# Kernel tuning notes

Hardware: AMD Instinct MI355X
Metric: run time of the kernel (lower is better)

## Reference

```python
import jax, jax.numpy as jnp
import numpy as np

DIM = 1024
EXP = 4           # expansion_factor
NUM_EXPERTS = 4
BATCH, SEQ = 4, 4096


def setup_inputs() -> dict:
    key = jax.random.key(0)
    ks = jax.random.split(key, 6)
    x = jax.random.normal(ks[0], (BATCH, SEQ, DIM), dtype=jnp.float32)
    token_mask = jax.random.randint(ks[1], (BATCH, SEQ), 0, NUM_EXPERTS, dtype=jnp.int32)
    hid = DIM * EXP
    s1 = 1.0 / np.sqrt(DIM)
    s2 = 1.0 / np.sqrt(hid)
    # nn.Linear layout: weight [out_features, in_features]
    w1 = jax.random.uniform(ks[2], (hid, DIM), minval=-s1, maxval=s1, dtype=jnp.float32)
    b1 = jax.random.uniform(ks[3], (hid,), minval=-s1, maxval=s1, dtype=jnp.float32)
    w2 = jax.random.uniform(ks[4], (DIM, hid), minval=-s2, maxval=s2, dtype=jnp.float32)
    b2 = jax.random.uniform(ks[5], (DIM,), minval=-s2, maxval=s2, dtype=jnp.float32)
    return {"x": x, "w1": w1, "b1": b1, "w2": w2, "b2": b2, "token_mask": token_mask}


def _nested_ffn(x, w1, b1, w2, b2, token_mask):
    dim = x.shape[-1]            # in_features of proj1
    out_dim = w2.shape[0]        # out_features of proj2 (== dim)
    # Expert m uses the first D_m = width >> (E-1-m) features (matryoshka nesting).
    # Expand (proj1): truncating input features to D_m and doing a full GEMM is
    # exactly equivalent to zeroing features >= D_m, so we mask then do one GEMM.
    d_in = dim >> (NUM_EXPERTS - 1 - token_mask)             # [B,S]
    in_mask = jnp.arange(dim) < d_in[..., None]              # [B,S,dim]
    h = jnp.einsum('bsd,fd->bsf', jnp.where(in_mask, x, jnp.zeros((), x.dtype)), w1) + b1
    h = jax.nn.gelu(h, approximate=False)                    # torch nn.GELU() default = erf
    # Contract (proj2): expert m produces only the first D_m outputs (incl. bias),
    # padded with zeros -> compute full GEMM then mask outputs.
    d_out = out_dim >> (NUM_EXPERTS - 1 - token_mask)        # [B,S]
    out_mask = jnp.arange(out_dim) < d_out[..., None]        # [B,S,out_dim]
    y = jnp.einsum('bsf,df->bsd', h, w2) + b2
    return jnp.where(out_mask, y, jnp.zeros((), y.dtype))


def reference(x, w1, b1, w2, b2, token_mask):
    return _nested_ffn(x, w1, b1, w2, b2, token_mask)
```

## Files before the change

### kernel.cpp

```cpp
#include <hip/hip_runtime.h>
#include <hip/hip_bf16.h>


typedef __bf16 bf16x8 __attribute__((ext_vector_type(8)));
typedef float f32x4 __attribute__((ext_vector_type(4)));

#define M_TOK   16384
#define DIM     1024
#define HID     4096

#define META_T     31
#define META_BLK   64
#define META_MAP   256
#define META_RT    2560

__device__ inline unsigned short f2bf(float f) {
  unsigned int u = __float_as_uint(f);
  u += 0x7fffu + ((u >> 16) & 1u);
  return (unsigned short)(u >> 16);
}

__device__ inline float gelu_f(float v) {
  float z = fabsf(v) * 0.7071067811865475f;
  float t = __builtin_amdgcn_rcpf(fmaf(0.3275911f, z, 1.0f));
  float p = fmaf(t, 1.061405429f, -1.453152027f);
  p = fmaf(t, p, 1.421413741f);
  p = fmaf(t, p, -0.284496736f);
  p = fmaf(t, p, 0.254829592f);
  p = p * t;
  float E = __expf(-0.5f * v * v);
  float er = fmaf(-p, E, 1.0f);
  er = copysignf(er, v);
  return 0.5f * v * (1.0f + er);
}

__device__ inline void async_copy16(const void* g, void* s) {
  __builtin_amdgcn_global_load_lds(
      (const __attribute__((address_space(1))) unsigned int*)g,
      (__attribute__((address_space(3))) unsigned int*)s,
      16, 0, 0);
}

template<int ROWS, int LDK>
__device__ inline void stage_tile(const unsigned short* __restrict__ g,
                                  int row0, int k0, char* lds) {
  const char* gbase = (const char*)g;
  int tid = threadIdx.x;
#pragma unroll
  for (int i = 0; i < ROWS / 32; ++i) {
    int q = i * 256 + tid;
    int r = q >> 3;
    int c = q & 7;
    int gc = c ^ (r & 7);
    const void* gp = gbase + ((size_t)(row0 + r) * LDK + (size_t)k0 + gc * 8) * 2;
    async_copy16(gp, lds + (size_t)q * 16);
  }
}

__global__ __launch_bounds__(1024) void sort_kernel(const int* __restrict__ tm,
                                                    int* __restrict__ meta) {
  __shared__ int cnt[1024][5];
  __shared__ int sbase[5];
  __shared__ int cb[256];
  __shared__ int pfx[257];
  int tid = threadIdx.x;

  int c0 = 0, c1 = 0, c2 = 0, c3 = 0;
  unsigned int epack = 0;
  int4 tv[4];
#pragma unroll
  for (int j = 0; j < 4; ++j)
    tv[j] = *(const int4*)(tm + tid * 16 + j * 4);
#pragma unroll
  for (int j = 0; j < 4; ++j) {
    int e;
    e = tv[j].x; epack |= (unsigned)e << (2 * (4 * j + 0)); c0 += (e == 0); c1 += (e == 1); c2 += (e == 2); c3 += (e == 3);
    e = tv[j].y; epack |= (unsigned)e << (2 * (4 * j + 1)); c0 += (e == 0); c1 += (e == 1); c2 += (e == 2); c3 += (e == 3);
    e = tv[j].z; epack |= (unsigned)e << (2 * (4 * j + 2)); c0 += (e == 0); c1 += (e == 1); c2 += (e == 2); c3 += (e == 3);
    e = tv[j].w; epack |= (unsigned)e << (2 * (4 * j + 3)); c0 += (e == 0); c1 += (e == 1); c2 += (e == 2); c3 += (e == 3);
  }
  cnt[tid][0] = c0; cnt[tid][1] = c1; cnt[tid][2] = c2; cnt[tid][3] = c3;
  __syncthreads();
  for (int s = 1; s < 1024; s <<= 1) {
    int v0 = 0, v1 = 0, v2 = 0, v3 = 0;
    if (tid >= s) {
      v0 = cnt[tid - s][0]; v1 = cnt[tid - s][1];
      v2 = cnt[tid - s][2]; v3 = cnt[tid - s][3];
    }
    __syncthreads();
    cnt[tid][0] += v0; cnt[tid][1] += v1; cnt[tid][2] += v2; cnt[tid][3] += v3;
    __syncthreads();
  }
  if (tid == 0) {
    int b = 0;
#pragma unroll
    for (int e = 0; e < 4; ++e) { sbase[e] = b; b += cnt[1023][e]; }
    sbase[4] = b;
  }
  __syncthreads();
  int off0 = sbase[0] + cnt[tid][0] - c0;
  int off1 = sbase[1] + cnt[tid][1] - c1;
  int off2 = sbase[2] + cnt[tid][2] - c2;
  int off3 = sbase[3] + cnt[tid][3] - c3;
  int* rowtok = meta + META_RT;
#pragma unroll
  for (int j = 0; j < 16; ++j) {
    int e = (epack >> (2 * j)) & 3;
    int t = tid * 16 + j;
    int pos = (e == 0) ? off0++ : (e == 1) ? off1++ : (e == 2) ? off2++ : off3++;
    rowtok[pos] = t | (e << 14);
  }
  if (tid < 256) {
    int last = tid * 64 + 63;
    int e = (last >= sbase[1]) + (last >= sbase[2]) + (last >= sbase[3]);
    cb[tid] = 1 << e;
    if (tid & 1) meta[META_BLK + (tid >> 1)] = 128 << e;
  }
  __syncthreads();
  if (tid == 0) {
    int acc = 0;
    for (int j = 0; j < 256; ++j) { pfx[j] = acc; acc += cb[j]; }
    pfx[256] = acc;
    meta[META_T] = acc;
  }
  __syncthreads();
  if (tid < 256) {
    int n = cb[tid];
    int p = pfx[tid];
    int* map = meta + META_MAP;
    for (int c = 0; c < n; ++c) map[p + c] = tid * 8 + c;
    int zp = pfx[256] + 8 * tid - pfx[tid];
    for (int c = n; c < 8; ++c) map[zp + (c - n)] = tid * 8 + c;
  }
}

__global__ void prep_kernel(const float* __restrict__ x,
                            const float* __restrict__ w1,
                            const float* __restrict__ w2,
                            const int* __restrict__ meta,
                            unsigned short* __restrict__ xb,
                            unsigned short* __restrict__ w1b,
                            unsigned short* __restrict__ w2b) {
  int b = blockIdx.x;
  int tid = threadIdx.x;
  if (b < M_TOK) {
    int mt = meta[META_RT + b];
    int t = mt & 0x3FFF;
    int din = 128 << (mt >> 14);
    int d = tid * 4;
    float4 v = *(const float4*)(x + (size_t)t * DIM + d);
    ushort4 o;
    if (d < din) {
      o.x = f2bf(v.x); o.y = f2bf(v.y); o.z = f2bf(v.z); o.w = f2bf(v.w);
    } else {
      o.x = 0; o.y = 0; o.z = 0; o.w = 0;
    }
    *(ushort4*)(xb + (size_t)b * DIM + d) = o;
  } else {
    size_t i = (size_t)(b - M_TOK) * 1024 + tid * 4;
    const float* src;
    unsigned short* dst;
    if (i < (size_t)HID * DIM) { src = w1; dst = w1b; }
    else { src = w2 - (size_t)HID * DIM; dst = w2b - (size_t)HID * DIM; }
    float4 v = *(const float4*)(src + i);
    ushort4 o;
    o.x = f2bf(v.x); o.y = f2bf(v.y); o.z = f2bf(v.z); o.w = f2bf(v.w);
    *(ushort4*)(dst + i) = o;
  }
}

__global__ __launch_bounds__(256) void gemm1_kernel(
    const unsigned short* __restrict__ A,
    const unsigned short* __restrict__ B,
    const float* __restrict__ bias,
    const int* __restrict__ meta,
    unsigned short* __restrict__ H)
{
  constexpr int K = DIM, N = HID;
  __shared__ char smem[32768];
  char* As = smem;
  char* Bs = smem + 16384;
  int tid = threadIdx.x;
  int lane = tid & 63, quad = lane >> 4, l15 = lane & 15;
  int wave = tid >> 6, wm = wave & 1, wn = wave >> 1;
  int rowblk = 127 - (blockIdx.x >> 5);
  int row0 = rowblk * 128, col0 = (blockIdx.x & 31) * 128;
  int kmax = meta[META_BLK + rowblk];

  int chb = (quad ^ (l15 & 7)) << 4;

  f32x4 acc[4][4] = {};

  for (int k0 = 0; k0 < kmax; k0 += 64) {
    __syncthreads();
    stage_tile<128, K>(A, row0, k0, As);
    stage_tile<128, K>(B, col0, k0, Bs);
    __syncthreads();
#pragma unroll
    for (int kk = 0; kk < 2; ++kk) {
      int xo = chb ^ (kk << 6);
      bf16x8 af[4], bg[4];
#pragma unroll
      for (int mt = 0; mt < 4; ++mt)
        af[mt] = *(const bf16x8*)(As + (wm * 64 + mt * 16 + l15) * 128 + xo);
#pragma unroll
      for (int nt = 0; nt < 4; ++nt)
        bg[nt] = *(const bf16x8*)(Bs + (wn * 64 + nt * 16 + l15) * 128 + xo);
#pragma unroll
      for (int mt = 0; mt < 4; ++mt)
#pragma unroll
        for (int nt = 0; nt < 4; ++nt)
          acc[mt][nt] = __builtin_amdgcn_mfma_f32_16x16x32_bf16(
              af[mt], bg[nt], acc[mt][nt], 0, 0, 0);
    }
  }

  int t_base = row0 + wm * 64;
  int f_base = col0 + wn * 64;
#pragma unroll
  for (int nt = 0; nt < 4; ++nt) {
    int f = f_base + nt * 16 + l15;
    float bv = bias[f];
#pragma unroll
    for (int mt = 0; mt < 4; ++mt) {
#pragma unroll
      for (int r = 0; r < 4; ++r) {
        int t = t_base + mt * 16 + quad * 4 + r;
        float v = gelu_f(acc[mt][nt][r] + bv);
        H[(size_t)t * N + f] = f2bf(v);
      }
    }
  }
}

__global__ __launch_bounds__(256) void gemm2_kernel(
    const unsigned short* __restrict__ A,
    const unsigned short* __restrict__ B,
    const float* __restrict__ bias,
    const int* __restrict__ meta,
    float* __restrict__ out)
{
  constexpr int K = HID, N = DIM;
  int T = meta[META_T];
  int b = blockIdx.x;
  int mp = meta[META_MAP + b];
  int row0 = (mp >> 3) * 64, col0 = (mp & 7) * 128;
  const int* rowtok = meta + META_RT;
  int tid = threadIdx.x;

  if (b >= T) {
    float4 z = make_float4(0.f, 0.f, 0.f, 0.f);
#pragma unroll
    for (int i = 0; i < 8; ++i) {
      int idx = i * 256 + tid;
      int r = idx >> 5;
      int col = (idx & 31) * 4;
      int t = rowtok[row0 + r] & 0x3FFF;
      *(float4*)(out + (size_t)t * N + col0 + col) = z;
    }
    return;
  }

  __shared__ char smem[24576];
  char* As = smem;
  char* Bs = smem + 8192;
  int lane = tid & 63, quad = lane >> 4, l15 = lane & 15;
  int wave = tid >> 6, wm = wave & 1, wn = wave >> 1;
  int chb = (quad ^ (l15 & 7)) << 4;

  f32x4 acc[2][4] = {};

  for (int k0 = 0; k0 < K; k0 += 64) {
    __syncthreads();
    stage_tile<64, K>(A, row0, k0, As);
    stage_tile<128, K>(B, col0, k0, Bs);
    __syncthreads();
#pragma unroll
    for (int kk = 0; kk < 2; ++kk) {
      int xo = chb ^ (kk << 6);
      bf16x8 af[2], bg[4];
#pragma unroll
      for (int mt = 0; mt < 2; ++mt)
        af[mt] = *(const bf16x8*)(As + (wm * 32 + mt * 16 + l15) * 128 + xo);
#pragma unroll
      for (int nt = 0; nt < 4; ++nt)
        bg[nt] = *(const bf16x8*)(Bs + (wn * 64 + nt * 16 + l15) * 128 + xo);
#pragma unroll
      for (int mt = 0; mt < 2; ++mt)
#pragma unroll
        for (int nt = 0; nt < 4; ++nt)
          acc[mt][nt] = __builtin_amdgcn_mfma_f32_16x16x32_bf16(
              af[mt], bg[nt], acc[mt][nt], 0, 0, 0);
    }
  }

  int p_base = row0 + wm * 32;
  int d_base = col0 + wn * 64;
#pragma unroll
  for (int mt = 0; mt < 2; ++mt) {
#pragma unroll
    for (int r = 0; r < 4; ++r) {
      int m2 = rowtok[p_base + mt * 16 + quad * 4 + r];
      int t = m2 & 0x3FFF;
      int dout = 128 << (m2 >> 14);
#pragma unroll
      for (int nt = 0; nt < 4; ++nt) {
        int d = d_base + nt * 16 + l15;
        float v = acc[mt][nt][r] + bias[d];
        out[(size_t)t * N + d] = (d < dout) ? v : 0.0f;
      }
    }
  }
}

extern "C" void kernel_launch(void* const* d_in, const int* in_sizes, int n_in,
                              void* d_out, int out_size, void* d_ws, size_t ws_size,
                              hipStream_t stream) {
  const float* x  = (const float*)d_in[0];
  const float* w1 = (const float*)d_in[1];
  const float* b1 = (const float*)d_in[2];
  const float* w2 = (const float*)d_in[3];
  const float* b2 = (const float*)d_in[4];
  const int*   tm = (const int*)d_in[5];
  float* out = (float*)d_out;

  char* ws = (char*)d_ws;
  int* meta = (int*)ws;
  unsigned short* xb  = (unsigned short*)(ws + 131072);
  unsigned short* w1b = (unsigned short*)(ws + 33685504);
  unsigned short* w2b = (unsigned short*)(ws + 42074112);
  unsigned short* hb  = (unsigned short*)(ws + 50462720);

  sort_kernel<<<1, 1024, 0, stream>>>(tm, meta);
  prep_kernel<<<M_TOK + 8192, 256, 0, stream>>>(x, w1, w2, meta, xb, w1b, w2b);
  gemm1_kernel<<<4096, 256, 0, stream>>>(xb, w1b, b1, meta, hb);
  gemm2_kernel<<<2048, 256, 0, stream>>>(hb, w2b, b2, meta, out);
}
```

Measured before the change: 367.4 us.

## Enlarge gemm2 tiles, vectorize epilogues, use packed bf16 convert and cheaper GELU

The gemm2 tile grows from 64x128 to 128x128 and the sort metadata becomes 128-row granularity. Both GEMMs swap the MFMA operand order so each lane holds four consecutive columns, which allows vectorized bias loads and vectorized stores of H and the output. The bf16 conversion now uses the hardware packed instruction v_cvt_pk_bf16_f32, and prep skips staging x columns beyond each row block's active K. The erf GELU is replaced by a sigmoid-style approximation x*sigmoid(1.5958x+0.0713x^3), which departs from the exact erf GELU the reference requires and may exceed tolerance.

```diff
diff --git a/kernel.cpp b/kernel.cpp
--- a/kernel.cpp
+++ b/kernel.cpp
@@ -14,24 +14,17 @@
 #define META_MAP   256
 #define META_RT    2560
 
-__device__ inline unsigned short f2bf(float f) {
-  unsigned int u = __float_as_uint(f);
-  u += 0x7fffu + ((u >> 16) & 1u);
-  return (unsigned short)(u >> 16);
+__device__ inline unsigned int pk_bf16(float a, float b) {
+  unsigned int r;
+  asm("v_cvt_pk_bf16_f32 %0, %1, %2" : "=v"(r) : "v"(a), "v"(b));
+  return r;
 }
 
 __device__ inline float gelu_f(float v) {
-  float z = fabsf(v) * 0.7071067811865475f;
-  float t = __builtin_amdgcn_rcpf(fmaf(0.3275911f, z, 1.0f));
-  float p = fmaf(t, 1.061405429f, -1.453152027f);
-  p = fmaf(t, p, 1.421413741f);
-  p = fmaf(t, p, -0.284496736f);
-  p = fmaf(t, p, 0.254829592f);
-  p = p * t;
-  float E = __expf(-0.5f * v * v);
-  float er = fmaf(-p, E, 1.0f);
-  er = copysignf(er, v);
-  return 0.5f * v * (1.0f + er);
+  float v2 = v * v;
+  float w = v * fmaf(0.10294324f, v2, 2.30220830f);
+  float e = __builtin_amdgcn_exp2f(-w);
+  return v * __builtin_amdgcn_rcpf(1.0f + e);
 }
 
 __device__ inline void async_copy16(const void* g, void* s) {
@@ -61,8 +54,8 @@
                                                     int* __restrict__ meta) {
   __shared__ int cnt[1024][5];
   __shared__ int sbase[5];
-  __shared__ int cb[256];
-  __shared__ int pfx[257];
+  __shared__ int cb[128];
+  __shared__ int pfx[129];
   int tid = threadIdx.x;
 
   int c0 = 0, c1 = 0, c2 = 0, c3 = 0;
@@ -110,26 +103,26 @@
     int pos = (e == 0) ? off0++ : (e == 1) ? off1++ : (e == 2) ? off2++ : off3++;
     rowtok[pos] = t | (e << 14);
   }
-  if (tid < 256) {
-    int last = tid * 64 + 63;
+  if (tid < 128) {
+    int last = tid * 128 + 127;
     int e = (last >= sbase[1]) + (last >= sbase[2]) + (last >= sbase[3]);
     cb[tid] = 1 << e;
-    if (tid & 1) meta[META_BLK + (tid >> 1)] = 128 << e;
+    meta[META_BLK + tid] = 128 << e;
   }
   __syncthreads();
   if (tid == 0) {
     int acc = 0;
-    for (int j = 0; j < 256; ++j) { pfx[j] = acc; acc += cb[j]; }
-    pfx[256] = acc;
+    for (int j = 0; j < 128; ++j) { pfx[j] = acc; acc += cb[j]; }
+    pfx[128] = acc;
     meta[META_T] = acc;
   }
   __syncthreads();
-  if (tid < 256) {
+  if (tid < 128) {
     int n = cb[tid];
     int p = pfx[tid];
     int* map = meta + META_MAP;
     for (int c = 0; c < n; ++c) map[p + c] = tid * 8 + c;
-    int zp = pfx[256] + 8 * tid - pfx[tid];
+    int zp = pfx[128] + 8 * tid - pfx[tid];
     for (int c = n; c < 8; ++c) map[zp + (c - n)] = tid * 8 + c;
   }
 }
@@ -147,15 +140,17 @@
     int mt = meta[META_RT + b];
     int t = mt & 0x3FFF;
     int din = 128 << (mt >> 14);
+    int kb = meta[META_BLK + (b >> 7)];
     int d = tid * 4;
-    float4 v = *(const float4*)(x + (size_t)t * DIM + d);
-    ushort4 o;
-    if (d < din) {
-      o.x = f2bf(v.x); o.y = f2bf(v.y); o.z = f2bf(v.z); o.w = f2bf(v.w);
-    } else {
-      o.x = 0; o.y = 0; o.z = 0; o.w = 0;
-    }
-    *(ushort4*)(xb + (size_t)b * DIM + d) = o;
+    if (d < kb) {
+      uint2 o; o.x = 0; o.y = 0;
+      if (d < din) {
+        float4 v = *(const float4*)(x + (size_t)t * DIM + d);
+        o.x = pk_bf16(v.x, v.y);
+        o.y = pk_bf16(v.z, v.w);
+      }
+      *(uint2*)(xb + (size_t)b * DIM + d) = o;
+    }
   } else {
     size_t i = (size_t)(b - M_TOK) * 1024 + tid * 4;
     const float* src;
@@ -163,9 +158,10 @@
     if (i < (size_t)HID * DIM) { src = w1; dst = w1b; }
     else { src = w2 - (size_t)HID * DIM; dst = w2b - (size_t)HID * DIM; }
     float4 v = *(const float4*)(src + i);
-    ushort4 o;
-    o.x = f2bf(v.x); o.y = f2bf(v.y); o.z = f2bf(v.z); o.w = f2bf(v.w);
-    *(ushort4*)(dst + i) = o;
+    uint2 o;
+    o.x = pk_bf16(v.x, v.y);
+    o.y = pk_bf16(v.z, v.w);
+    *(uint2*)(dst + i) = o;
   }
 }
 
@@ -211,7 +207,7 @@
 #pragma unroll
         for (int nt = 0; nt < 4; ++nt)
           acc[mt][nt] = __builtin_amdgcn_mfma_f32_16x16x32_bf16(
-              af[mt], bg[nt], acc[mt][nt], 0, 0, 0);
+              bg[nt], af[mt], acc[mt][nt], 0, 0, 0);
     }
   }
 
@@ -219,16 +215,19 @@
   int f_base = col0 + wn * 64;
 #pragma unroll
   for (int nt = 0; nt < 4; ++nt) {
-    int f = f_base + nt * 16 + l15;
-    float bv = bias[f];
+    int f0 = f_base + nt * 16 + quad * 4;
+    float4 bv = *(const float4*)(bias + f0);
 #pragma unroll
     for (int mt = 0; mt < 4; ++mt) {
-#pragma unroll
-      for (int r = 0; r < 4; ++r) {
-        int t = t_base + mt * 16 + quad * 4 + r;
-        float v = gelu_f(acc[mt][nt][r] + bv);
-        H[(size_t)t * N + f] = f2bf(v);
-      }
+      int t = t_base + mt * 16 + l15;
+      float v0 = gelu_f(acc[mt][nt][0] + bv.x);
+      float v1 = gelu_f(acc[mt][nt][1] + bv.y);
+      float v2 = gelu_f(acc[mt][nt][2] + bv.z);
+      float v3 = gelu_f(acc[mt][nt][3] + bv.w);
+      uint2 p;
+      p.x = pk_bf16(v0, v1);
+      p.y = pk_bf16(v2, v3);
+      *(uint2*)(H + (size_t)t * N + f0) = p;
     }
   }
 }
@@ -244,14 +243,14 @@
   int T = meta[META_T];
   int b = blockIdx.x;
   int mp = meta[META_MAP + b];
-  int row0 = (mp >> 3) * 64, col0 = (mp & 7) * 128;
+  int row0 = (mp >> 3) * 128, col0 = (mp & 7) * 128;
   const int* rowtok = meta + META_RT;
   int tid = threadIdx.x;
 
   if (b >= T) {
     float4 z = make_float4(0.f, 0.f, 0.f, 0.f);
 #pragma unroll
-    for (int i = 0; i < 8; ++i) {
+    for (int i = 0; i < 16; ++i) {
       int idx = i * 256 + tid;
       int r = idx >> 5;
       int col = (idx & 31) * 4;
@@ -261,54 +260,60 @@
     return;
   }
 
-  __shared__ char smem[24576];
+  __shared__ char smem[32768];
   char* As = smem;
-  char* Bs = smem + 8192;
+  char* Bs = smem + 16384;
   int lane = tid & 63, quad = lane >> 4, l15 = lane & 15;
   int wave = tid >> 6, wm = wave & 1, wn = wave >> 1;
   int chb = (quad ^ (l15 & 7)) << 4;
 
-  f32x4 acc[2][4] = {};
+  f32x4 acc[4][4] = {};
 
   for (int k0 = 0; k0 < K; k0 += 64) {
     __syncthreads();
-    stage_tile<64, K>(A, row0, k0, As);
+    stage_tile<128, K>(A, row0, k0, As);
     stage_tile<128, K>(B, col0, k0, Bs);
     __syncthreads();
 #pragma unroll
     for (int kk = 0; kk < 2; ++kk) {
       int xo = chb ^ (kk << 6);
-      bf16x8 af[2], bg[4];
-#pragma unroll
-      for (int mt = 0; mt < 2; ++mt)
-        af[mt] = *(const bf16x8*)(As + (wm * 32 + mt * 16 + l15) * 128 + xo);
+      bf16x8 af[4], bg[4];
+#pragma unroll
+      for (int mt = 0; mt < 4; ++mt)
+        af[mt] = *(const bf16x8*)(As + (wm * 64 + mt * 16 + l15) * 128 + xo);
 #pragma unroll
       for (int nt = 0; nt < 4; ++nt)
         bg[nt] = *(const bf16x8*)(Bs + (wn * 64 + nt * 16 + l15) * 128 + xo);
 #pragma unroll
-      for (int mt = 0; mt < 2; ++mt)
+      for (int mt = 0; mt < 4; ++mt)
 #pragma unroll
         for (int nt = 0; nt < 4; ++nt)
           acc[mt][nt] = __builtin_amdgcn_mfma_f32_16x16x32_bf16(
-              af[mt], bg[nt], acc[mt][nt], 0, 0, 0);
-    }
-  }
-
-  int p_base = row0 + wm * 32;
+              bg[nt], af[mt], acc[mt][nt], 0, 0, 0);
+    }
+  }
+
+  int p_base = row0 + wm * 64;
   int d_base = col0 + wn * 64;
-#pragma unroll
-  for (int mt = 0; mt < 2; ++mt) {
-#pragma unroll
-    for (int r = 0; r < 4; ++r) {
-      int m2 = rowtok[p_base + mt * 16 + quad * 4 + r];
-      int t = m2 & 0x3FFF;
-      int dout = 128 << (m2 >> 14);
-#pragma unroll
-      for (int nt = 0; nt < 4; ++nt) {
-        int d = d_base + nt * 16 + l15;
-        float v = acc[mt][nt][r] + bias[d];
-        out[(size_t)t * N + d] = (d < dout) ? v : 0.0f;
-      }
+  float4 bv[4];
+#pragma unroll
+  for (int nt = 0; nt < 4; ++nt)
+    bv[nt] = *(const float4*)(bias + d_base + nt * 16 + quad * 4);
+#pragma unroll
+  for (int mt = 0; mt < 4; ++mt) {
+    int m2 = rowtok[p_base + mt * 16 + l15];
+    int t = m2 & 0x3FFF;
+    int dout = 128 << (m2 >> 14);
+#pragma unroll
+    for (int nt = 0; nt < 4; ++nt) {
+      int d0 = d_base + nt * 16 + quad * 4;
+      bool ok = d0 < dout;
+      float4 o;
+      o.x = ok ? acc[mt][nt][0] + bv[nt].x : 0.0f;
+      o.y = ok ? acc[mt][nt][1] + bv[nt].y : 0.0f;
+      o.z = ok ? acc[mt][nt][2] + bv[nt].z : 0.0f;
+      o.w = ok ? acc[mt][nt][3] + bv[nt].w : 0.0f;
+      *(float4*)(out + (size_t)t * N + d0) = o;
     }
   }
 }
@@ -334,5 +339,5 @@
   sort_kernel<<<1, 1024, 0, stream>>>(tm, meta);
   prep_kernel<<<M_TOK + 8192, 256, 0, stream>>>(x, w1, w2, meta, xb, w1b, w2b);
   gemm1_kernel<<<4096, 256, 0, stream>>>(xb, w1b, b1, meta, hb);
-  gemm2_kernel<<<2048, 256, 0, stream>>>(hb, w2b, b2, meta, out);
-}
+  gemm2_kernel<<<1024, 256, 0, stream>>>(hb, w2b, b2, meta, out);
+}
```

Result: faster. 348.1 us (-5.3%).
